# Kernel optimization log

Hardware: AMD Instinct MI355X
Metric: run time of the kernel (lower is better)

Reference implementation:

```python
import jax, jax.numpy as jnp
import numpy as np


def _rot_mat(thetas, scales):
    # thetas, scales: [bs, g] -> [bs, g, 9, 9] bilinear-interpolation matrices
    bs, g = thetas.shape
    t = thetas.reshape(-1)
    s = scales.reshape(-1)
    x = jnp.cos(t) * s
    y = jnp.sin(t) * s
    yp = -y
    z = jnp.zeros_like(x)
    o = jnp.ones_like(x)
    a = x - y; b = x * y; c = x + y; d = a * c; e = a + c
    ap = x - yp; bp = x * yp; cp = x + yp; dp = ap * cp; ep = ap + cp

    def M(rows):
        # rows: 9 lists of 9 [N]-arrays -> [9, 9, N]
        return jnp.stack([jnp.stack(r, axis=0) for r in rows], axis=0)

    ctr = [z, z, z, z, o, z, z, z, z]

    pb1 = M([
        [a, 1 - a, z, z, z, z, z, z, z],
        [z, 1 - y, y, z, z, z, z, z, z],
        [z, z, a, z, z, 1 - a, z, z, z],
        [y, z, z, 1 - y, z, z, z, z, z],
        ctr,
        [z, z, z, z, z, 1 - y, z, z, y],
        [z, z, z, 1 - a, z, z, a, z, z],
        [z, z, z, z, z, z, y, 1 - y, z],
        [z, z, z, z, z, z, z, 1 - a, a]])
    pb2 = M([
        [a, 1 - a, z, z, z, z, z, z, z],
        [z, x - b, b, z, 1 - c + b, y - b, z, z, z],
        [z, z, a, z, z, 1 - a, z, z, z],
        [b, y - b, z, x - b, 1 - c + b, z, z, z, z],
        ctr,
        [z, z, z, z, 1 - c + b, x - b, z, y - b, b],
        [z, z, z, 1 - a, z, z, a, z, z],
        [z, z, z, y - b, 1 - c + b, z, b, x - b, z],
        [z, z, z, z, z, z, z, 1 - a, a]])
    ps1 = M([
        [d, a - d, z, c - d, 1 - e + d, z, z, z, z],
        [z, x - b, b, z, 1 - c + b, y - b, z, z, z],
        [z, c - d, d, z, 1 - e + d, a - d, z, z, z],
        [b, y - b, z, x - b, 1 - c + b, z, z, z, z],
        ctr,
        [z, z, z, z, 1 - c + b, x - b, z, y - b, b],
        [z, z, z, a - d, 1 - e + d, z, d, c - d, z],
        [z, z, z, y - b, 1 - c + b, z, b, x - b, z],
        [z, z, z, z, 1 - e + d, c - d, z, a - d, d]])
    ps2 = pb2  # identical in the source
    nb1 = M([
        [cp, z, z, 1 - cp, z, z, z, z, z],
        [yp, 1 - yp, z, z, z, z, z, z, z],
        [z, 1 - cp, cp, z, z, z, z, z, z],
        [z, z, z, 1 - yp, z, z, yp, z, z],
        ctr,
        [z, z, yp, z, z, 1 - yp, z, z, z],
        [z, z, z, z, z, z, cp, 1 - cp, z],
        [z, z, z, z, z, z, z, 1 - yp, yp],
        [z, z, z, z, z, 1 - cp, z, z, cp]])
    nb2 = M([
        [cp, z, z, 1 - cp, z, z, z, z, z],
        [bp, x - bp, z, yp - bp, 1 - cp + bp, z, z, z, z],
        [z, 1 - cp, cp, z, z, z, z, z, z],
        [z, z, z, x - bp, 1 - cp + bp, z, bp, yp - bp, z],
        ctr,
        [z, yp - bp, bp, z, 1 - cp + bp, x - bp, z, z, z],
        [z, z, z, z, z, z, cp, 1 - cp, z],
        [z, z, z, z, 1 - cp + bp, yp - bp, z, x - bp, bp],
        [z, z, z, z, z, 1 - cp, z, z, cp]])
    ns1 = M([
        [dp, cp - dp, z, ap - dp, 1 - ep + dp, z, z, z, z],
        [bp, x - bp, z, yp - bp, 1 - cp + bp, z, z, z, z],
        [z, ap - dp, dp, z, 1 - ep + dp, cp - dp, z, z, z],
        [z, yp - bp, bp, z, 1 - cp + bp, x - bp, z, z, z],
        ctr,
        [z, z, z, x - bp, 1 - cp + bp, z, bp, yp - bp, z],
        [z, z, z, cp - dp, 1 - ep + dp, z, dp, ap - dp, z],
        [z, z, z, z, 1 - cp + bp, yp - bp, z, x - bp, bp],
        [z, z, z, z, 1 - ep + dp, ap - dp, z, cp - dp, dp]])
    ns2 = nb2  # mirrors the positive branch where small_2 == big_2

    m_pos = (t >= 0.0)[None, None, :]
    m_big = (s >= 1.0)[None, None, :]
    m_1 = (jnp.abs(t) <= jnp.pi / 4)[None, None, :]
    pos = jnp.where(m_big, jnp.where(m_1, pb1, pb2), jnp.where(m_1, ps1, ps2))
    neg = jnp.where(m_big, jnp.where(m_1, nb1, nb2), jnp.where(m_1, ns1, ns2))
    rot = jnp.where(m_pos, pos, neg)  # [9, 9, bs*g]
    return jnp.transpose(rot, (2, 0, 1)).reshape(bs, g, 9, 9)


def _forward(x, thetas, scales, lambdas, weight):
    # x: [B, Cin, H, W]; weight: [n, Cout, Cin, 3, 3]; thetas/scales/lambdas: [B, n]
    B, Cin, H, W = x.shape
    n, Cout = weight.shape[0], weight.shape[1]
    rot = _rot_mat(thetas, scales) * lambdas[:, :, None, None]  # [B, n, 9, 9]
    w9 = weight.reshape(n, Cout, Cin, 9)
    # per-sample transformed kernel: sum over kernel_number n and source taps j
    w = jnp.einsum('bnij,nocj->bioc', rot, w9)  # [B, 9, Cout, Cin]
    w = jnp.transpose(w, (0, 2, 3, 1)).reshape(B * Cout, Cin, 3, 3)
    xg = x.reshape(1, B * Cin, H, W)
    out = jax.lax.conv_general_dilated(
        xg, w, window_strides=(1, 1), padding=((1, 1), (1, 1)),
        dimension_numbers=('NCHW', 'OIHW', 'NCHW'), feature_group_count=B)
    return out.reshape(B, Cout, H, W)


def setup_inputs() -> dict:
    key = jax.random.key(0)
    ks = jax.random.split(key, 5)
    B, Cin, Cout, H, W, n = 16, 256, 256, 64, 64, 4
    x = jax.random.normal(ks[0], (B, Cin, H, W), dtype=jnp.float32)
    thetas = jax.random.uniform(ks[1], (B, n), minval=-1.2, maxval=1.2, dtype=jnp.float32)
    scales = jax.random.uniform(ks[2], (B, n), minval=0.5, maxval=1.5, dtype=jnp.float32)
    lambdas = jax.nn.softmax(jax.random.normal(ks[3], (B, n), dtype=jnp.float32), axis=-1)
    weight = jax.random.normal(ks[4], (n, Cout, Cin, 3, 3), dtype=jnp.float32) * 0.05
    return {"x": x, "thetas": thetas, "scales": scales, "lambdas": lambdas, "weight": weight}


def reference(x, thetas, scales, lambdas, weight):
    return _forward(x, thetas, scales, lambdas, weight)
```

## Files before the change

### kernel.cpp

```cpp
#include <hip/hip_runtime.h>
#include <cstdint>
#include <cstddef>

typedef unsigned short ushort_t;
typedef __attribute__((ext_vector_type(4))) float f32x4;
typedef __attribute__((ext_vector_type(8))) short s16x8;

#define PI_4F 0.78539816339744830962f

__device__ inline ushort_t f2bf(float f) {
  unsigned int u = __float_as_uint(f);
  u = u + 0x7fffu + ((u >> 16) & 1u);
  return (ushort_t)(u >> 16);
}

__device__ void rot_compute(float t, float s, float* M) {
  float xv = cosf(t) * s, yv = sinf(t) * s;
  bool pos = (t >= 0.0f), big = (s >= 1.0f), m1 = (fabsf(t) <= PI_4F);
#pragma unroll
  for (int i = 0; i < 81; ++i) M[i] = 0.0f;
  M[36 + 4] = 1.0f;
  if (pos) {
    float a = xv - yv, bb = xv * yv, c = xv + yv;
    if (m1 && big) {
      M[0] = a; M[1] = 1 - a;
      M[9 + 1] = 1 - yv; M[9 + 2] = yv;
      M[18 + 2] = a; M[18 + 5] = 1 - a;
      M[27 + 0] = yv; M[27 + 3] = 1 - yv;
      M[45 + 5] = 1 - yv; M[45 + 8] = yv;
      M[54 + 3] = 1 - a; M[54 + 6] = a;
      M[63 + 6] = yv; M[63 + 7] = 1 - yv;
      M[72 + 7] = 1 - a; M[72 + 8] = a;
    } else if (m1) {
      float d = a * c, e = a + c;
      M[0] = d; M[1] = a - d; M[3] = c - d; M[4] = 1 - e + d;
      M[9 + 1] = xv - bb; M[9 + 2] = bb; M[9 + 4] = 1 - c + bb; M[9 + 5] = yv - bb;
      M[18 + 1] = c - d; M[18 + 2] = d; M[18 + 4] = 1 - e + d; M[18 + 5] = a - d;
      M[27 + 0] = bb; M[27 + 1] = yv - bb; M[27 + 3] = xv - bb; M[27 + 4] = 1 - c + bb;
      M[45 + 4] = 1 - c + bb; M[45 + 5] = xv - bb; M[45 + 7] = yv - bb; M[45 + 8] = bb;
      M[54 + 3] = a - d; M[54 + 4] = 1 - e + d; M[54 + 6] = d; M[54 + 7] = c - d;
      M[63 + 3] = yv - bb; M[63 + 4] = 1 - c + bb; M[63 + 6] = bb; M[63 + 7] = xv - bb;
      M[72 + 4] = 1 - e + d; M[72 + 5] = c - d; M[72 + 7] = a - d; M[72 + 8] = d;
    } else {
      M[0] = a; M[1] = 1 - a;
      M[9 + 1] = xv - bb; M[9 + 2] = bb; M[9 + 4] = 1 - c + bb; M[9 + 5] = yv - bb;
      M[18 + 2] = a; M[18 + 5] = 1 - a;
      M[27 + 0] = bb; M[27 + 1] = yv - bb; M[27 + 3] = xv - bb; M[27 + 4] = 1 - c + bb;
      M[45 + 4] = 1 - c + bb; M[45 + 5] = xv - bb; M[45 + 7] = yv - bb; M[45 + 8] = bb;
      M[54 + 3] = 1 - a; M[54 + 6] = a;
      M[63 + 3] = yv - bb; M[63 + 4] = 1 - c + bb; M[63 + 6] = bb; M[63 + 7] = xv - bb;
      M[72 + 7] = 1 - a; M[72 + 8] = a;
    }
  } else {
    float yp = -yv;
    float ap = xv - yp, bp = xv * yp, cp = xv + yp;
    if (m1 && big) {
      M[0] = cp; M[3] = 1 - cp;
      M[9 + 0] = yp; M[9 + 1] = 1 - yp;
      M[18 + 1] = 1 - cp; M[18 + 2] = cp;
      M[27 + 3] = 1 - yp; M[27 + 6] = yp;
      M[45 + 2] = yp; M[45 + 5] = 1 - yp;
      M[54 + 6] = cp; M[54 + 7] = 1 - cp;
      M[63 + 7] = 1 - yp; M[63 + 8] = yp;
      M[72 + 5] = 1 - cp; M[72 + 8] = cp;
    } else if (m1) {
      float dp = ap * cp, ep = ap + cp;
      M[0] = dp; M[1] = cp - dp; M[3] = ap - dp; M[4] = 1 - ep + dp;
      M[9 + 0] = bp; M[9 + 1] = xv - bp; M[9 + 3] = yp - bp; M[9 + 4] = 1 - cp + bp;
      M[18 + 1] = ap - dp; M[18 + 2] = dp; M[18 + 4] = 1 - ep + dp; M[18 + 5] = cp - dp;
      M[27 + 1] = yp - bp; M[27 + 2] = bp; M[27 + 4] = 1 - cp + bp; M[27 + 5] = xv - bp;
      M[45 + 3] = xv - bp; M[45 + 4] = 1 - cp + bp; M[45 + 6] = bp; M[45 + 7] = yp - bp;
      M[54 + 3] = cp - dp; M[54 + 4] = 1 - ep + dp; M[54 + 6] = dp; M[54 + 7] = ap - dp;
      M[63 + 4] = 1 - cp + bp; M[63 + 5] = yp - bp; M[63 + 7] = xv - bp; M[63 + 8] = bp;
      M[72 + 4] = 1 - ep + dp; M[72 + 5] = ap - dp; M[72 + 7] = cp - dp; M[72 + 8] = dp;
    } else {
      M[0] = cp; M[3] = 1 - cp;
      M[9 + 0] = bp; M[9 + 1] = xv - bp; M[9 + 3] = yp - bp; M[9 + 4] = 1 - cp + bp;
      M[18 + 1] = 1 - cp; M[18 + 2] = cp;
      M[27 + 3] = xv - bp; M[27 + 4] = 1 - cp + bp; M[27 + 6] = bp; M[27 + 7] = yp - bp;
      M[45 + 1] = yp - bp; M[45 + 2] = bp; M[45 + 4] = 1 - cp + bp; M[45 + 5] = xv - bp;
      M[54 + 6] = cp; M[54 + 7] = 1 - cp;
      M[63 + 4] = 1 - cp + bp; M[63 + 5] = yp - bp; M[63 + 7] = xv - bp; M[63 + 8] = bp;
      M[72 + 5] = 1 - cp; M[72 + 8] = cp;
    }
  }
}

__global__ __launch_bounds__(256) void prep_kernel(
    const float* __restrict__ x, const float* __restrict__ weight,
    const float* __restrict__ thetas, const float* __restrict__ scales,
    const float* __restrict__ lambdas, ushort_t* __restrict__ xpad,
    ushort_t* __restrict__ wtout) {
  __shared__ __align__(16) char smem[32 * 81 * 4];
  const int bi = blockIdx.x;
  const int t = threadIdx.x;

  if (bi < 256) {
    float* rotl = (float*)smem;
    const int o2 = bi & 127, bq = bi >> 7;
    const int half = t >> 7, tloc = t & 127;
    const int o = o2 * 2 + half;
    const int c = tloc * 2;
    float wv0[4][9], wv1[4][9];
#pragma unroll
    for (int n = 0; n < 4; ++n) {
      const float* wp = weight + (((size_t)(n * 256 + o)) * 256 + c) * 9;
#pragma unroll
      for (int j = 0; j < 9; ++j) { wv0[n][j] = wp[j]; wv1[n][j] = wp[9 + j]; }
    }
    if (t < 32) {
      int gid = bq * 32 + t;
      float M[81];
      rot_compute(thetas[gid], scales[gid], M);
      float lam = lambdas[gid];
#pragma unroll
      for (int i = 0; i < 81; ++i) rotl[t * 81 + i] = M[i] * lam;
    }
    __syncthreads();
#pragma unroll
    for (int bl = 0; bl < 8; ++bl) {
      const int b = bq * 8 + bl;
#pragma unroll
      for (int i = 0; i < 9; ++i) {
        float a0 = 0.0f, a1 = 0.0f;
#pragma unroll
        for (int n = 0; n < 4; ++n) {
          const float* r = &rotl[(bl * 4 + n) * 81 + i * 9];
#pragma unroll
          for (int j = 0; j < 9; ++j) {
            a0 = fmaf(r[j], wv0[n][j], a0);
            a1 = fmaf(r[j], wv1[n][j], a1);
          }
        }
        unsigned int word = (unsigned int)f2bf(a0) | ((unsigned int)f2bf(a1) << 16);
        *(unsigned int*)&wtout[((size_t)((b * 9 + i) * 256 + o)) * 256 + c] = word;
      }
    }
  } else {
    ushort_t (*tile)[68] = (ushort_t(*)[68])smem;
    const int bi2 = bi - 256;
    const int b = bi2 >> 8, ct = (bi2 >> 6) & 3, st = bi2 & 63;
    const int c0 = ct * 64;
    const float* xb = x + ((size_t)(b * 256 + c0)) * 4096 + st * 64;
#pragma unroll
    for (int k = 0; k < 4; ++k) {
      int idx = t + 256 * k;
      int c_l = idx >> 4, w4 = (idx & 15) * 4;
      float4 v = *(const float4*)&xb[(size_t)c_l * 4096 + w4];
      tile[w4 + 0][c_l] = f2bf(v.x);
      tile[w4 + 1][c_l] = f2bf(v.y);
      tile[w4 + 2][c_l] = f2bf(v.z);
      tile[w4 + 3][c_l] = f2bf(v.w);
    }
    __syncthreads();
    const int c4 = (t & 15) * 4, wl = t >> 4;
    const size_t rowbase = (size_t)(b * 4356 + (st + 1) * 66) * 256 + c0;
#pragma unroll
    for (int k = 0; k < 4; ++k) {
      int w = wl + 16 * k;
      uint2 v = *(const uint2*)&tile[w][c4];
      *(uint2*)&xpad[rowbase + (size_t)(w + 1) * 256 + c4] = v;
    }
    if (t < 32) {
      int w = (t & 16) ? 65 : 0;
      int cc = (t & 15) * 4;
      *(uint2*)&xpad[rowbase + (size_t)w * 256 + cc] = make_uint2(0u, 0u);
    }
    if (st == 0 || st == 63) {
      const int h = (st == 0) ? 0 : 65;
      const size_t hb = (size_t)(b * 4356 + h * 66) * 256 + c0;
      for (int idx = t; idx < 66 * 16; idx += 256) {
        int w = idx >> 4, cc = (idx & 15) * 4;
        *(uint2*)&xpad[hb + (size_t)w * 256 + cc] = make_uint2(0u, 0u);
      }
    }
  }
}

__device__ inline void gload16(const ushort_t* g, ushort_t* l) {
  __builtin_amdgcn_global_load_lds(
      (const __attribute__((address_space(1))) unsigned int*)g,
      (__attribute__((address_space(3))) unsigned int*)l, 16, 0, 0);
}

#define WAITB(N)                                                      \
  asm volatile("s_waitcnt vmcnt(" #N ") lgkmcnt(0)\n\ts_barrier" ::: "memory")

__global__ __launch_bounds__(512, 2) void conv_kernel(
    const ushort_t* __restrict__ xpad, const ushort_t* __restrict__ wt,
    float* __restrict__ out) {
  __shared__ __align__(16) ushort_t As0[8192], As1[8192], As2[8192];
  __shared__ __align__(16) ushort_t Bs0[8192], Bs1[8192], Bs2[8192];

  const int id = blockIdx.x;
  const int xcd = id & 7;
  const int jj = id >> 3;
  const int b = xcd * 2 + (jj >> 4);
  const int ntile = jj & 15;

  const int t = threadIdx.x;
  const int wave = t >> 6, lane = t & 63;
  const int wm = wave & 1, wn = wave >> 1;
  const int lr = lane & 15, lq = lane >> 4;
  const int h0 = ntile * 4;

  const ushort_t* wt_b = wt + (size_t)b * 589824;
  const ushort_t* xp_b = xpad + (size_t)b * 1115136;

  const int lrow = t >> 2;
  const int cg8 = (((t & 3) ^ ((t >> 3) & 3)) * 8);
  const int rsw = (lr >> 1) & 3;
  const int aoff = (wm * 128 + lr) * 32 + ((lq ^ rsw) * 8);
  const int boff = (wn * 64 + lr) * 32 + ((lq ^ rsw) * 8);

  f32x4 acc[8][4];
#pragma unroll
  for (int i = 0; i < 8; ++i)
#pragma unroll
    for (int j2 = 0; j2 < 4; ++j2) acc[i][j2] = (f32x4)(0.0f);

  auto stage = [&](int ks, ushort_t* Ad, ushort_t* Bd) {
    const int tap = ks >> 3;
    const int c0k = (ks & 7) << 5;
    const int kh = tap / 3, kw = tap - kh * 3;
    const ushort_t* ga = wt_b + ((size_t)(tap * 256 + lrow)) * 256 + c0k + cg8;
    gload16(ga, Ad + wave * 512);
    gload16(ga + 128 * 256, Ad + 4096 + wave * 512);
    const int sp = (h0 + (lrow >> 6) + kh) * 66 + kw + (lrow & 63);
    gload16(xp_b + (size_t)sp * 256 + c0k + cg8, Bd + wave * 512);
    gload16(xp_b + (size_t)(sp + 132) * 256 + c0k + cg8, Bd + 4096 + wave * 512);
  };

  auto compute = [&](const ushort_t* Ab, const ushort_t* Bb) {
    s16x8 bfr[4];
#pragma unroll
    for (int ni = 0; ni < 4; ++ni)
      bfr[ni] = *(const s16x8*)(Bb + boff + ni * 512);
#pragma unroll
    for (int mi = 0; mi < 8; ++mi) {
      s16x8 af = *(const s16x8*)(Ab + aoff + mi * 512);
#pragma unroll
      for (int ni = 0; ni < 4; ++ni)
        acc[mi][ni] = __builtin_amdgcn_mfma_f32_16x16x32_bf16(af, bfr[ni], acc[mi][ni], 0, 0, 0);
    }
  };

  stage(0, As0, Bs0);
  stage(1, As1, Bs1);

#pragma unroll 1
  for (int kk = 0; kk < 23; ++kk) {
    const int ks = kk * 3;
    WAITB(4);
    stage(ks + 2, As2, Bs2);
    compute(As0, Bs0);
    WAITB(4);
    stage(ks + 3, As0, Bs0);
    compute(As1, Bs1);
    WAITB(4);
    stage(ks + 4, As1, Bs1);
    compute(As2, Bs2);
  }
  WAITB(4);
  stage(71, As2, Bs2);
  compute(As0, Bs0);
  WAITB(4);
  compute(As1, Bs1);
  WAITB(0);
  compute(As2, Bs2);

  float* ob = out + ((size_t)(b * 256 + wm * 128)) * 4096 + ntile * 256 + wn * 64 + lr;
#pragma unroll
  for (int mi = 0; mi < 8; ++mi)
#pragma unroll
    for (int r = 0; r < 4; ++r) {
      float* orow = ob + (size_t)(mi * 16 + lq * 4 + r) * 4096;
#pragma unroll
      for (int ni = 0; ni < 4; ++ni) orow[ni * 16] = acc[mi][ni][r];
    }
}

extern "C" void kernel_launch(void* const* d_in, const int* in_sizes, int n_in,
                              void* d_out, int out_size, void* d_ws, size_t ws_size,
                              hipStream_t stream) {
  const float* x = (const float*)d_in[0];
  const float* thetas = (const float*)d_in[1];
  const float* scales = (const float*)d_in[2];
  const float* lambdas = (const float*)d_in[3];
  const float* weight = (const float*)d_in[4];
  float* out = (float*)d_out;

  ushort_t* wt_ws = (ushort_t*)d_ws;
  ushort_t* xpad_ws = (ushort_t*)((char*)d_ws + 18874368);

  prep_kernel<<<4352, 256, 0, stream>>>(x, weight, thetas, scales, lambdas,
                                        xpad_ws, wt_ws);
  conv_kernel<<<256, 512, 0, stream>>>(xpad_ws, wt_ws, out);
}
```

Measured before the change: 205.4 us.

## Restructure conv GEMM main loop into ping-pong 4-buffer schedule with split stages

Replaces the three-buffer LDS pipeline with four A and four B buffers, splitting each k-step into two 32-channel halves. A and B global-to-LDS loads are issued separately and interleaved between half-MFMA groups. Each group is fenced with barriers, s_setprio, and sched_barrier to overlap memory with compute. LDS use grows from 96KB to 128KB per block, which may reduce occupancy under launch_bounds(512,2), and the added barriers add synchronisation cost.

```diff
diff --git a/kernel.cpp b/kernel.cpp
--- a/kernel.cpp
+++ b/kernel.cpp
@@ -183,14 +183,45 @@
       (__attribute__((address_space(3))) unsigned int*)l, 16, 0, 0);
 }
 
-#define WAITB(N)                                                      \
-  asm volatile("s_waitcnt vmcnt(" #N ") lgkmcnt(0)\n\ts_barrier" ::: "memory")
+#define GROUP(ACUR, BCUR, S1, S2, VN)                                          \
+  do {                                                                         \
+    s16x8 bfr[4], afr[4];                                                      \
+    _Pragma("unroll") for (int ni = 0; ni < 4; ++ni)                           \
+        bfr[ni] = *(const s16x8*)(BCUR + boff + ni * 512);                     \
+    _Pragma("unroll") for (int m = 0; m < 4; ++m)                              \
+        afr[m] = *(const s16x8*)(ACUR + aoff + m * 512);                       \
+    S1;                                                                        \
+    __builtin_amdgcn_s_barrier();                                              \
+    asm volatile("s_waitcnt lgkmcnt(0)" ::: "memory");                         \
+    __builtin_amdgcn_sched_barrier(0);                                         \
+    __builtin_amdgcn_s_setprio(1);                                             \
+    _Pragma("unroll") for (int m = 0; m < 4; ++m)                              \
+        _Pragma("unroll") for (int ni = 0; ni < 4; ++ni)                       \
+            acc[m][ni] = __builtin_amdgcn_mfma_f32_16x16x32_bf16(              \
+                afr[m], bfr[ni], acc[m][ni], 0, 0, 0);                         \
+    __builtin_amdgcn_s_setprio(0);                                             \
+    __builtin_amdgcn_s_barrier();                                              \
+    _Pragma("unroll") for (int m = 0; m < 4; ++m)                              \
+        afr[m] = *(const s16x8*)(ACUR + aoff + (4 + m) * 512);                 \
+    S2;                                                                        \
+    __builtin_amdgcn_s_barrier();                                              \
+    asm volatile("s_waitcnt lgkmcnt(0)" ::: "memory");                         \
+    __builtin_amdgcn_sched_barrier(0);                                         \
+    __builtin_amdgcn_s_setprio(1);                                             \
+    _Pragma("unroll") for (int m = 0; m < 4; ++m)                              \
+        _Pragma("unroll") for (int ni = 0; ni < 4; ++ni)                       \
+            acc[4 + m][ni] = __builtin_amdgcn_mfma_f32_16x16x32_bf16(          \
+                afr[m], bfr[ni], acc[4 + m][ni], 0, 0, 0);                     \
+    __builtin_amdgcn_s_setprio(0);                                             \
+    asm volatile("s_waitcnt vmcnt(" #VN ")" ::: "memory");                     \
+    __builtin_amdgcn_s_barrier();                                              \
+  } while (0)
 
 __global__ __launch_bounds__(512, 2) void conv_kernel(
     const ushort_t* __restrict__ xpad, const ushort_t* __restrict__ wt,
     float* __restrict__ out) {
-  __shared__ __align__(16) ushort_t As0[8192], As1[8192], As2[8192];
-  __shared__ __align__(16) ushort_t Bs0[8192], Bs1[8192], Bs2[8192];
+  __shared__ __align__(16) ushort_t A00[8192], A01[8192], A10[8192], A11[8192];
+  __shared__ __align__(16) ushort_t B00[8192], B01[8192], B10[8192], B11[8192];
 
   const int id = blockIdx.x;
   const int xcd = id & 7;
@@ -219,55 +250,42 @@
 #pragma unroll
     for (int j2 = 0; j2 < 4; ++j2) acc[i][j2] = (f32x4)(0.0f);
 
-  auto stage = [&](int ks, ushort_t* Ad, ushort_t* Bd) {
-    const int tap = ks >> 3;
-    const int c0k = (ks & 7) << 5;
-    const int kh = tap / 3, kw = tap - kh * 3;
+  auto stage_A = [&](int k, int c, ushort_t* Ad) {
+    const int tap = k >> 2;
+    const int c0k = ((k & 3) << 6) + (c << 5);
     const ushort_t* ga = wt_b + ((size_t)(tap * 256 + lrow)) * 256 + c0k + cg8;
     gload16(ga, Ad + wave * 512);
     gload16(ga + 128 * 256, Ad + 4096 + wave * 512);
+  };
+  auto stage_B = [&](int k, int c, ushort_t* Bd) {
+    const int tap = k >> 2;
+    const int c0k = ((k & 3) << 6) + (c << 5);
+    const int kh = tap / 3, kw = tap - kh * 3;
     const int sp = (h0 + (lrow >> 6) + kh) * 66 + kw + (lrow & 63);
     gload16(xp_b + (size_t)sp * 256 + c0k + cg8, Bd + wave * 512);
     gload16(xp_b + (size_t)(sp + 132) * 256 + c0k + cg8, Bd + 4096 + wave * 512);
   };
 
-  auto compute = [&](const ushort_t* Ab, const ushort_t* Bb) {
-    s16x8 bfr[4];
-#pragma unroll
-    for (int ni = 0; ni < 4; ++ni)
-      bfr[ni] = *(const s16x8*)(Bb + boff + ni * 512);
-#pragma unroll
-    for (int mi = 0; mi < 8; ++mi) {
-      s16x8 af = *(const s16x8*)(Ab + aoff + mi * 512);
-#pragma unroll
-      for (int ni = 0; ni < 4; ++ni)
-        acc[mi][ni] = __builtin_amdgcn_mfma_f32_16x16x32_bf16(af, bfr[ni], acc[mi][ni], 0, 0, 0);
-    }
-  };
-
-  stage(0, As0, Bs0);
-  stage(1, As1, Bs1);
+  stage_A(0, 0, A00);
+  stage_B(0, 0, B00);
+  stage_A(0, 1, A01);
+  stage_B(0, 1, B01);
+  stage_A(1, 0, A10);
+  asm volatile("s_waitcnt vmcnt(6)" ::: "memory");
+  __builtin_amdgcn_s_barrier();
 
 #pragma unroll 1
-  for (int kk = 0; kk < 23; ++kk) {
-    const int ks = kk * 3;
-    WAITB(4);
-    stage(ks + 2, As2, Bs2);
-    compute(As0, Bs0);
-    WAITB(4);
-    stage(ks + 3, As0, Bs0);
-    compute(As1, Bs1);
-    WAITB(4);
-    stage(ks + 4, As1, Bs1);
-    compute(As2, Bs2);
+  for (int i = 0; i < 17; ++i) {
+    const int k0 = 2 * i;
+    GROUP(A00, B00, stage_B(k0 + 1, 0, B10), stage_A(k0 + 1, 1, A11), 6);
+    GROUP(A01, B01, stage_B(k0 + 1, 1, B11), stage_A(k0 + 2, 0, A00), 6);
+    GROUP(A10, B10, stage_B(k0 + 2, 0, B00), stage_A(k0 + 2, 1, A01), 6);
+    GROUP(A11, B11, stage_B(k0 + 2, 1, B01), stage_A(k0 + 3, 0, A10), 6);
   }
-  WAITB(4);
-  stage(71, As2, Bs2);
-  compute(As0, Bs0);
-  WAITB(4);
-  compute(As1, Bs1);
-  WAITB(0);
-  compute(As2, Bs2);
+  GROUP(A00, B00, stage_B(35, 0, B10), stage_A(35, 1, A11), 6);
+  GROUP(A01, B01, stage_B(35, 1, B11), ((void)0), 4);
+  GROUP(A10, B10, ((void)0), ((void)0), 0);
+  GROUP(A11, B11, ((void)0), ((void)0), 0);
 
   float* ob = out + ((size_t)(b * 256 + wm * 128)) * 4096 + ntile * 256 + wn * 64 + lr;
 #pragma unroll
```

New measurement: 213.4 us. 1.04x slower.

## Double-buffer MFMA fragments in registers and interleave with explicit schedule groups

Applied to the files above, without the earlier changes.

Reorganises the conv GEMM main loop so that LDS fragments for the next k-step are loaded into a second register set while MFMAs run on the current set. Three global-to-LDS stages are issued before the loop. The loop runs a uniform 72 steps, with out-of-range stages clamped to re-load step 71. sched_group_barrier hints interleave the VMEM, DS reads and MFMAs. The aim is to hide LDS read latency behind the matrix ops, at the cost of many more live fragment registers (spill or occupancy risk) and a few redundant tail loads.

```diff
diff --git a/kernel.cpp b/kernel.cpp
--- a/kernel.cpp
+++ b/kernel.cpp
@@ -186,6 +186,16 @@
 #define WAITB(N)                                                      \
   asm volatile("s_waitcnt vmcnt(" #N ") lgkmcnt(0)\n\ts_barrier" ::: "memory")
 
+#define STEP(KS3, AN, BN, AD, BD, AFC, BFC, AFN, BFN)                 \
+  WAITB(4);                                                           \
+  __builtin_amdgcn_sched_barrier(0);                                  \
+  stage((KS3) > 71 ? 71 : (KS3), AD, BD);                             \
+  fragload(AN, BN, AFN, BFN);                                         \
+  mfma_step(AFC, BFC);                                                \
+  __builtin_amdgcn_sched_group_barrier(0x020, 4, 0);   \
+  __builtin_amdgcn_sched_group_barrier(0x100, 12, 0);   \
+  __builtin_amdgcn_sched_group_barrier(0x008, 32, 0);
+
 __global__ __launch_bounds__(512, 2) void conv_kernel(
     const ushort_t* __restrict__ xpad, const ushort_t* __restrict__ wt,
     float* __restrict__ out) {
@@ -218,6 +228,8 @@
   for (int i = 0; i < 8; ++i)
 #pragma unroll
     for (int j2 = 0; j2 < 4; ++j2) acc[i][j2] = (f32x4)(0.0f);
+
+  s16x8 afA[8], bfA[4], afB[8], bfB[4];
 
   auto stage = [&](int ks, ushort_t* Ad, ushort_t* Bd) {
     const int tap = ks >> 3;
@@ -231,43 +243,38 @@
     gload16(xp_b + (size_t)(sp + 132) * 256 + c0k + cg8, Bd + 4096 + wave * 512);
   };
 
-  auto compute = [&](const ushort_t* Ab, const ushort_t* Bb) {
-    s16x8 bfr[4];
-#pragma unroll
-    for (int ni = 0; ni < 4; ++ni)
-      bfr[ni] = *(const s16x8*)(Bb + boff + ni * 512);
-#pragma unroll
-    for (int mi = 0; mi < 8; ++mi) {
-      s16x8 af = *(const s16x8*)(Ab + aoff + mi * 512);
+  auto fragload = [&](const ushort_t* Ab, const ushort_t* Bb, s16x8* af, s16x8* bf) {
+#pragma unroll
+    for (int ni = 0; ni < 4; ++ni) bf[ni] = *(const s16x8*)(Bb + boff + ni * 512);
+#pragma unroll
+    for (int mi = 0; mi < 8; ++mi) af[mi] = *(const s16x8*)(Ab + aoff + mi * 512);
+  };
+
+  auto mfma_step = [&](const s16x8* af, const s16x8* bf) {
+#pragma unroll
+    for (int mi = 0; mi < 8; ++mi)
 #pragma unroll
       for (int ni = 0; ni < 4; ++ni)
-        acc[mi][ni] = __builtin_amdgcn_mfma_f32_16x16x32_bf16(af, bfr[ni], acc[mi][ni], 0, 0, 0);
-    }
+        acc[mi][ni] = __builtin_amdgcn_mfma_f32_16x16x32_bf16(af[mi], bf[ni], acc[mi][ni], 0, 0, 0);
   };
 
   stage(0, As0, Bs0);
   stage(1, As1, Bs1);
+  stage(2, As2, Bs2);
+  asm volatile("s_waitcnt vmcnt(4)" ::: "memory");
+  __builtin_amdgcn_s_barrier();
+  fragload(As0, Bs0, afA, bfA);
 
 #pragma unroll 1
-  for (int kk = 0; kk < 23; ++kk) {
-    const int ks = kk * 3;
-    WAITB(4);
-    stage(ks + 2, As2, Bs2);
-    compute(As0, Bs0);
-    WAITB(4);
-    stage(ks + 3, As0, Bs0);
-    compute(As1, Bs1);
-    WAITB(4);
-    stage(ks + 4, As1, Bs1);
-    compute(As2, Bs2);
+  for (int kk = 0; kk < 12; ++kk) {
+    const int ks = kk * 6;
+    STEP(ks + 3, As1, Bs1, As0, Bs0, afA, bfA, afB, bfB);
+    STEP(ks + 4, As2, Bs2, As1, Bs1, afB, bfB, afA, bfA);
+    STEP(ks + 5, As0, Bs0, As2, Bs2, afA, bfA, afB, bfB);
+    STEP(ks + 6, As1, Bs1, As0, Bs0, afB, bfB, afA, bfA);
+    STEP(ks + 7, As2, Bs2, As1, Bs1, afA, bfA, afB, bfB);
+    STEP(ks + 8, As0, Bs0, As2, Bs2, afB, bfB, afA, bfA);
   }
-  WAITB(4);
-  stage(71, As2, Bs2);
-  compute(As0, Bs0);
-  WAITB(4);
-  compute(As1, Bs1);
-  WAITB(0);
-  compute(As2, Bs2);
 
   float* ob = out + ((size_t)(b * 256 + wm * 128)) * 4096 + ntile * 256 + wn * 64 + lr;
 #pragma unroll
```

Measured after the change: 243.3 us. 1.18x slower.
